# Optimization experiments

Measured on AMD Instinct MI355X. Metric: run time of the kernel, lower is better.

## Reference

```python
import jax, jax.numpy as jnp
import numpy as np

K = 8          # number of nearest neighbors (init kwarg k)
CONST = 0.1    # inverseweight const
NUM = 1.0      # inverseweight num


def setup_inputs() -> dict:
    key = jax.random.key(0)
    k1, k2 = jax.random.split(key)
    data1 = jax.random.normal(k1, (4096, 1024), dtype=jnp.float32)
    data2 = jax.random.normal(k2, (8192, 1024), dtype=jnp.float32)
    return {"data1": data1, "data2": data2}


def reference(data1, data2):
    # pairwise Euclidean distance (torch.dist with p=2): [N, M]
    x2 = jnp.sum(data1 * data1, axis=1, keepdims=True)          # [N, 1]
    y2 = jnp.sum(data2 * data2, axis=1)                         # [M]
    d2 = x2 + y2[None, :] - 2.0 * (data1 @ data2.T)             # [N, M]
    dist = jnp.sqrt(jnp.maximum(d2, 1e-12))

    # k smallest distances and their indices
    neg_top, idx = jax.lax.top_k(-dist, K)                      # [N, K]
    knn_dist = -neg_top                                         # [N, K]

    # inverse weighting: w = num / (dist + const)
    w = NUM / (knn_dist + CONST)                                # [N, K]

    # gather neighbor vectors and weighted-average them
    neigh = data2[idx]                                          # [N, K, D]
    out = jnp.einsum('nk,nkd->nd', w, neigh) / jnp.sum(w, axis=1, keepdims=True)
    return out
```

## Files before the change

kernel.cpp:

```cpp
#include <hip/hip_runtime.h>


typedef short bf16x8 __attribute__((ext_vector_type(8)));
typedef float f32x4 __attribute__((ext_vector_type(4)));

#define SENTINEL 1e30f
#define BKK 32

static __device__ __forceinline__ unsigned short f2bf(float f) {
  unsigned u = __float_as_uint(f);
  return (unsigned short)((u + 0x7fffu + ((u >> 16) & 1u)) >> 16);
}

__global__ __launch_bounds__(256) void convert_all_kernel(
    const float* __restrict__ A, const float* __restrict__ B,
    unsigned short* __restrict__ Abf, unsigned short* __restrict__ Bbf,
    float* __restrict__ y2, int N) {
  const int bid = blockIdx.x;
  const int tid = threadIdx.x;
  if (bid < N) {
    const float4 v = ((const float4*)&A[(size_t)bid * 1024])[tid];
    ushort4 o;
    o.x = f2bf(v.x); o.y = f2bf(v.y); o.z = f2bf(v.z); o.w = f2bf(v.w);
    ((ushort4*)&Abf[(size_t)bid * 1024])[tid] = o;
  } else {
    const int m = bid - N;
    __shared__ float red[256];
    const float4 v = ((const float4*)&B[(size_t)m * 1024])[tid];
    ushort4 o;
    o.x = f2bf(v.x); o.y = f2bf(v.y); o.z = f2bf(v.z); o.w = f2bf(v.w);
    ((ushort4*)&Bbf[(size_t)m * 1024])[tid] = o;
    red[tid] = v.x * v.x + v.y * v.y + v.z * v.z + v.w * v.w;
    __syncthreads();
    for (int s = 128; s > 0; s >>= 1) {
      if (tid < s) red[tid] += red[tid + s];
      __syncthreads();
    }
    if (tid == 0) y2[m] = red[0];
  }
}

#define CAS(sa, ia, sb, ib)                         \
  do {                                              \
    if ((sa) > (sb)) {                              \
      const float _t = (sa); (sa) = (sb); (sb) = _t;\
      const int _u = (ia); (ia) = (ib); (ib) = _u;  \
    }                                               \
  } while (0)

#define STAGE(sk, b)                                                          \
  do {                                                                        \
    const unsigned short* gA_ =                                               \
        Abf + (size_t)(r0 + w * 16 + srow) * 1024 + (sk) * 32 + sofs;         \
    const unsigned short* gB_ =                                               \
        Bbf + (size_t)(c0 + w * 32 + srow) * 1024 + (sk) * 32 + sofs;         \
    __builtin_amdgcn_global_load_lds(                                         \
        (const __attribute__((address_space(1))) void*)gA_,                   \
        (__attribute__((address_space(3))) void*)&As[b][(w * 16) * 32],       \
        16, 0, 0);                                                            \
    __builtin_amdgcn_global_load_lds(                                         \
        (const __attribute__((address_space(1))) void*)gB_,                   \
        (__attribute__((address_space(3))) void*)&Bs[b][(w * 32) * 32],       \
        16, 0, 0);                                                            \
    __builtin_amdgcn_global_load_lds(                                         \
        (const __attribute__((address_space(1))) void*)(gB_ + (size_t)16 * 1024), \
        (__attribute__((address_space(3))) void*)&Bs[b][(w * 32 + 16) * 32],  \
        16, 0, 0);                                                            \
  } while (0)

#define COMPUTE(b)                                                            \
  do {                                                                        \
    bf16x8 af, bfr[8];                                                        \
    af = *(const bf16x8*)&As[b][frowA * 32 + fofs];                           \
    _Pragma("unroll")                                                         \
    for (int fj = 0; fj < 8; ++fj)                                            \
      bfr[fj] = *(const bf16x8*)&Bs[b][(frowB + fj * 16) * 32 + fofs];        \
    __builtin_amdgcn_s_setprio(1);                                            \
    _Pragma("unroll")                                                         \
    for (int fj = 0; fj < 8; ++fj)                                            \
      acc[fj] = __builtin_amdgcn_mfma_f32_16x16x32_bf16(                      \
          bfr[fj], af, acc[fj], 0, 0, 0);                                     \
    __builtin_amdgcn_s_setprio(0);                                            \
  } while (0)

#define PIPE_SYNC(N)                                                          \
  do {                                                                        \
    asm volatile("s_waitcnt vmcnt(" #N ")" ::: "memory");                     \
    __builtin_amdgcn_sched_barrier(0);                                        \
    __builtin_amdgcn_s_barrier();                                             \
    __builtin_amdgcn_sched_barrier(0);                                        \
  } while (0)

__global__ __launch_bounds__(256, 4) void screen8_kernel(
    const unsigned short* __restrict__ Abf, const unsigned short* __restrict__ Bbf,
    const float* __restrict__ y2g,
    float* __restrict__ cand_s, int* __restrict__ cand_i) {
  __shared__ unsigned short As[3][64 * 32];
  __shared__ unsigned short Bs[3][128 * 32];

  const int tid = threadIdx.x;
  const int w = tid >> 6;
  const int lane = tid & 63;

  const int v = blockIdx.x + gridDim.x * blockIdx.y;
  const int u = v >> 3;
  const int window = (v & 7) * 8 + (u & 7);
  const int rowtile = u >> 3;
  const int r0 = rowtile * 64;
  const int c0 = window * 128;

  const int srow = lane >> 2;
  const int sofs = ((lane & 3) ^ ((lane >> 3) & 3)) * 8;

  const int frowA = w * 16 + (lane & 15);
  const int frowB = lane & 15;
  const int fofs = ((lane >> 4) ^ ((lane >> 1) & 3)) * 8;
  const int cgrp = (lane >> 4) * 4;

  f32x4 acc[8];
#pragma unroll
  for (int fj = 0; fj < 8; ++fj) {
    f32x4 z = {0.f, 0.f, 0.f, 0.f};
    acc[fj] = z;
  }

  STAGE(0, 0);
  STAGE(1, 1);
  int cA = 0, cB = 1, cC = 2;
  for (int t = 0; t < 31; ++t) {
    PIPE_SYNC(3);
    if (t < 30) STAGE(t + 2, cC);
    __builtin_amdgcn_sched_barrier(0);
    COMPUTE(cA);
    const int tmp = cA; cA = cB; cB = cC; cC = tmp;
  }
  PIPE_SYNC(0);
  COMPUTE(cA);

  float ls[8];
  int li[8];
#pragma unroll
  for (int j = 0; j < 8; ++j) { ls[j] = SENTINEL; li[j] = 0x7fffffff; }
  const int cb = c0 + cgrp;
#pragma unroll
  for (int fj = 0; fj < 8; ++fj) {
    const float4 y2q = *(const float4*)&y2g[c0 + fj * 16 + cgrp];
#pragma unroll
    for (int reg = 0; reg < 4; ++reg) {
      const float s = y2q[reg] - 2.0f * acc[fj][reg];
      if (s < ls[7]) {
        ls[7] = s; li[7] = cb + fj * 16 + reg;
#pragma unroll
        for (int j = 7; j > 0; --j) {
          if (ls[j] < ls[j - 1]) {
            const float t = ls[j]; ls[j] = ls[j - 1]; ls[j - 1] = t;
            const int u2 = li[j]; li[j] = li[j - 1]; li[j - 1] = u2;
          }
        }
      }
    }
  }
#pragma unroll
  for (int off = 16; off <= 32; off <<= 1) {
    float rs[8];
    int ri[8];
#pragma unroll
    for (int j = 0; j < 8; ++j) {
      rs[j] = __shfl_xor(ls[j], off, 64);
      ri[j] = __shfl_xor(li[j], off, 64);
    }
    float ms[8];
    int mi_[8];
#pragma unroll
    for (int i = 0; i < 8; ++i) {
      const bool t = ls[i] < rs[7 - i];
      ms[i] = t ? ls[i] : rs[7 - i];
      mi_[i] = t ? li[i] : ri[7 - i];
    }
    CAS(ms[0], mi_[0], ms[4], mi_[4]);
    CAS(ms[1], mi_[1], ms[5], mi_[5]);
    CAS(ms[2], mi_[2], ms[6], mi_[6]);
    CAS(ms[3], mi_[3], ms[7], mi_[7]);
    CAS(ms[0], mi_[0], ms[2], mi_[2]);
    CAS(ms[1], mi_[1], ms[3], mi_[3]);
    CAS(ms[4], mi_[4], ms[6], mi_[6]);
    CAS(ms[5], mi_[5], ms[7], mi_[7]);
    CAS(ms[0], mi_[0], ms[1], mi_[1]);
    CAS(ms[2], mi_[2], ms[3], mi_[3]);
    CAS(ms[4], mi_[4], ms[5], mi_[5]);
    CAS(ms[6], mi_[6], ms[7], mi_[7]);
#pragma unroll
    for (int j = 0; j < 8; ++j) { ls[j] = ms[j]; li[j] = mi_[j]; }
  }
  if ((lane >> 4) == 0) {
    const int row = r0 + w * 16 + lane;
    const size_t base = ((size_t)row * 64 + window) * 8;
#pragma unroll
    for (int j = 0; j < 8; ++j) {
      cand_s[base + j] = ls[j];
      cand_i[base + j] = li[j];
    }
  }
}

__global__ __launch_bounds__(256) void finalize6_kernel(
    const float* __restrict__ A, const float* __restrict__ B,
    const float* __restrict__ y2g,
    const float* __restrict__ cand_s, const int* __restrict__ cand_i,
    float* __restrict__ out) {
  const int tid = threadIdx.x;
  const int w = tid >> 6;
  const int lane = tid & 63;
  const int rloc = w >> 1;
  const int wh = w & 1;
  const int n = blockIdx.x * 2 + rloc;
  __shared__ float comb[2][2][16];

  float s12[12];
  int i12[12];
  {
    const float4* cs = (const float4*)&cand_s[(size_t)n * 512 + lane * 8];
    const int4* cj = (const int4*)&cand_i[(size_t)n * 512 + lane * 8];
    const float4 sa = cs[0], sb = cs[1];
    const int4 ja = cj[0], jb = cj[1];
    s12[0] = sa.x; s12[1] = sa.y; s12[2] = sa.z; s12[3] = sa.w;
    s12[4] = sb.x; s12[5] = sb.y; s12[6] = sb.z; s12[7] = sb.w;
    i12[0] = ja.x; i12[1] = ja.y; i12[2] = ja.z; i12[3] = ja.w;
    i12[4] = jb.x; i12[5] = jb.y; i12[6] = jb.z; i12[7] = jb.w;
#pragma unroll
    for (int j = 8; j < 12; ++j) { s12[j] = SENTINEL; i12[j] = 0x7fffffff; }
  }

#pragma unroll
  for (int off = 1; off <= 32; off <<= 1) {
    float rs[12];
    int ri[12];
#pragma unroll
    for (int j = 0; j < 12; ++j) {
      rs[j] = __shfl_xor(s12[j], off, 64);
      ri[j] = __shfl_xor(i12[j], off, 64);
    }
    float ms[12];
    int mj[12];
#pragma unroll
    for (int j = 0; j < 12; ++j) {
      const bool tke = s12[j] < rs[11 - j];
      ms[j] = tke ? s12[j] : rs[11 - j];
      mj[j] = tke ? i12[j] : ri[11 - j];
    }
    CAS(ms[0], mj[0], ms[8], mj[8]);  CAS(ms[1], mj[1], ms[9], mj[9]);
    CAS(ms[2], mj[2], ms[10], mj[10]); CAS(ms[3], mj[3], ms[11], mj[11]);
    CAS(ms[4], mj[4], ms[8], mj[8]);  CAS(ms[5], mj[5], ms[9], mj[9]);
    CAS(ms[6], mj[6], ms[10], mj[10]); CAS(ms[7], mj[7], ms[11], mj[11]);
    CAS(ms[0], mj[0], ms[2], mj[2]);  CAS(ms[1], mj[1], ms[3], mj[3]);
    CAS(ms[4], mj[4], ms[6], mj[6]);  CAS(ms[5], mj[5], ms[7], mj[7]);
    CAS(ms[8], mj[8], ms[10], mj[10]); CAS(ms[9], mj[9], ms[11], mj[11]);
    CAS(ms[0], mj[0], ms[1], mj[1]);  CAS(ms[2], mj[2], ms[3], mj[3]);
    CAS(ms[4], mj[4], ms[5], mj[5]);  CAS(ms[6], mj[6], ms[7], mj[7]);
    CAS(ms[8], mj[8], ms[9], mj[9]);  CAS(ms[10], mj[10], ms[11], mj[11]);
#pragma unroll
    for (int j = 0; j < 12; ++j) { s12[j] = ms[j]; i12[j] = mj[j]; }
  }

  const float4* Arow = (const float4*)&A[(size_t)n * 1024];
  const int fbase = wh * 128 + lane * 2;
  float4 a4[2];
  a4[0] = Arow[fbase];
  a4[1] = Arow[fbase + 1];
  float4 bk0[12], bk1[12];
#pragma unroll
  for (int j = 0; j < 12; ++j) {
    const float4* Brow = (const float4*)&B[(size_t)i12[j] * 1024];
    bk0[j] = Brow[fbase];
    bk1[j] = Brow[fbase + 1];
  }
  float part[13];
  part[12] = a4[0].x * a4[0].x + a4[0].y * a4[0].y + a4[0].z * a4[0].z +
             a4[0].w * a4[0].w + a4[1].x * a4[1].x + a4[1].y * a4[1].y +
             a4[1].z * a4[1].z + a4[1].w * a4[1].w;
#pragma unroll
  for (int j = 0; j < 12; ++j) {
    part[j] = a4[0].x * bk0[j].x + a4[0].y * bk0[j].y + a4[0].z * bk0[j].z +
              a4[0].w * bk0[j].w;
    part[j] += a4[1].x * bk1[j].x + a4[1].y * bk1[j].y + a4[1].z * bk1[j].z +
               a4[1].w * bk1[j].w;
  }
#pragma unroll
  for (int r = 0; r < 13; ++r) {
#pragma unroll
    for (int off = 32; off >= 1; off >>= 1) part[r] += __shfl_xor(part[r], off, 64);
  }
  if (lane == 0) {
#pragma unroll
    for (int r = 0; r < 13; ++r) comb[rloc][wh][r] = part[r];
  }
  __syncthreads();
  float tot[13];
#pragma unroll
  for (int r = 0; r < 13; ++r) tot[r] = comb[rloc][0][r] + comb[rloc][1][r];

  const float x2 = tot[12];
  float d2v[12];
  float wsel[12];
  bool used[12];
#pragma unroll
  for (int j = 0; j < 12; ++j) {
    d2v[j] = x2 + y2g[i12[j]] - 2.0f * tot[j];
    used[j] = false;
    wsel[j] = 0.0f;
  }
  float wsum = 0.0f;
  for (int k = 0; k < 8; ++k) {
    float bd = SENTINEL;
    int bi = 0x7fffffff, bslot = 0;
#pragma unroll
    for (int j = 0; j < 12; ++j) {
      if (used[j]) continue;
      const float d2 = d2v[j];
      if (d2 < bd || (d2 == bd && i12[j] < bi)) { bd = d2; bi = i12[j]; bslot = j; }
    }
    used[bslot] = true;
    const float d2c = fmaxf(bd, 1e-12f);
    const float wv = 1.0f / (sqrtf(d2c) + 0.1f);
    wsel[bslot] = wv;
    wsum += wv;
  }
  const float inv = 1.0f / wsum;

  float4 o0 = {0, 0, 0, 0}, o1 = {0, 0, 0, 0};
#pragma unroll
  for (int j = 0; j < 12; ++j) {
    const float wv = wsel[j];
    o0.x += wv * bk0[j].x; o0.y += wv * bk0[j].y;
    o0.z += wv * bk0[j].z; o0.w += wv * bk0[j].w;
    o1.x += wv * bk1[j].x; o1.y += wv * bk1[j].y;
    o1.z += wv * bk1[j].z; o1.w += wv * bk1[j].w;
  }
  o0.x *= inv; o0.y *= inv; o0.z *= inv; o0.w *= inv;
  o1.x *= inv; o1.y *= inv; o1.z *= inv; o1.w *= inv;
  float4* Orow = (float4*)&out[(size_t)n * 1024];
  Orow[fbase] = o0;
  Orow[fbase + 1] = o1;
}

__global__ __launch_bounds__(256) void rownorm_kernel(
    const float* __restrict__ B, float* __restrict__ y2) {
  const int m = blockIdx.x;
  const int tid = threadIdx.x;
  __shared__ float red[256];
  const float4 v = *(const float4*)&B[(size_t)m * 1024 + tid * 4];
  red[tid] = v.x * v.x + v.y * v.y + v.z * v.z + v.w * v.w;
  __syncthreads();
  for (int s = 128; s > 0; s >>= 1) {
    if (tid < s) red[tid] += red[tid + s];
    __syncthreads();
  }
  if (tid == 0) y2[m] = red[0];
}

__global__ __launch_bounds__(256) void knn_chunk_kernel(
    const float* __restrict__ A, const float* __restrict__ B,
    const float* __restrict__ y2g,
    float* __restrict__ cand_s, int* __restrict__ cand_i) {
  __shared__ float As[BKK][68];
  __shared__ float Bs[BKK][68];
  __shared__ float Sc[64][65];

  const int tid = threadIdx.x;
  const int tx = tid & 15;
  const int ty = tid >> 4;
  const int r0 = blockIdx.y * 64;
  const int c0 = blockIdx.x * 1024;
  const int lrow = tid >> 3;
  const int lk = (tid & 7) * 4;

  float top_s[8];
  int top_i[8];
#pragma unroll
  for (int j = 0; j < 8; ++j) { top_s[j] = SENTINEL; top_i[j] = 0x7fffffff; }

  for (int tile = 0; tile < 16; ++tile) {
    const int cbase = c0 + tile * 64;
    float acc[4][4];
#pragma unroll
    for (int i = 0; i < 4; ++i)
#pragma unroll
      for (int j = 0; j < 4; ++j) acc[i][j] = 0.0f;

    for (int k0 = 0; k0 < 1024; k0 += BKK) {
      const float4 a0 = *(const float4*)&A[(size_t)(r0 + lrow) * 1024 + k0 + lk];
      const float4 a1 = *(const float4*)&A[(size_t)(r0 + lrow + 32) * 1024 + k0 + lk];
      const float4 b0 = *(const float4*)&B[(size_t)(cbase + lrow) * 1024 + k0 + lk];
      const float4 b1 = *(const float4*)&B[(size_t)(cbase + lrow + 32) * 1024 + k0 + lk];
      __syncthreads();
      As[lk + 0][lrow] = a0.x; As[lk + 1][lrow] = a0.y;
      As[lk + 2][lrow] = a0.z; As[lk + 3][lrow] = a0.w;
      As[lk + 0][lrow + 32] = a1.x; As[lk + 1][lrow + 32] = a1.y;
      As[lk + 2][lrow + 32] = a1.z; As[lk + 3][lrow + 32] = a1.w;
      Bs[lk + 0][lrow] = b0.x; Bs[lk + 1][lrow] = b0.y;
      Bs[lk + 2][lrow] = b0.z; Bs[lk + 3][lrow] = b0.w;
      Bs[lk + 0][lrow + 32] = b1.x; Bs[lk + 1][lrow + 32] = b1.y;
      Bs[lk + 2][lrow + 32] = b1.z; Bs[lk + 3][lrow + 32] = b1.w;
      __syncthreads();
#pragma unroll
      for (int kk = 0; kk < BKK; ++kk) {
        const float4 av = *(const float4*)&As[kk][ty * 4];
        const float4 bv = *(const float4*)&Bs[kk][tx * 4];
        acc[0][0] += av.x * bv.x; acc[0][1] += av.x * bv.y;
        acc[0][2] += av.x * bv.z; acc[0][3] += av.x * bv.w;
        acc[1][0] += av.y * bv.x; acc[1][1] += av.y * bv.y;
        acc[1][2] += av.y * bv.z; acc[1][3] += av.y * bv.w;
        acc[2][0] += av.z * bv.x; acc[2][1] += av.z * bv.y;
        acc[2][2] += av.z * bv.z; acc[2][3] += av.z * bv.w;
        acc[3][0] += av.w * bv.x; acc[3][1] += av.w * bv.y;
        acc[3][2] += av.w * bv.z; acc[3][3] += av.w * bv.w;
      }
    }
#pragma unroll
    for (int i = 0; i < 4; ++i) {
      const int row = ty * 4 + i;
#pragma unroll
      for (int j = 0; j < 4; ++j) {
        const int col = tx * 4 + j;
        Sc[row][col] = y2g[cbase + col] - 2.0f * acc[i][j];
      }
    }
    __syncthreads();
    if (tid < 64) {
      for (int c = 0; c < 64; ++c) {
        const float s = Sc[tid][c];
        if (s < top_s[7]) {
          top_s[7] = s; top_i[7] = cbase + c;
#pragma unroll
          for (int j = 7; j > 0; --j) {
            if (top_s[j] < top_s[j - 1]) {
              const float tss = top_s[j]; top_s[j] = top_s[j - 1]; top_s[j - 1] = tss;
              const int tii = top_i[j]; top_i[j] = top_i[j - 1]; top_i[j - 1] = tii;
            }
          }
        }
      }
    }
  }

  if (tid < 64) {
    const int n = r0 + tid;
    const int base = (n * gridDim.x + blockIdx.x) * 8;
#pragma unroll
    for (int j = 0; j < 8; ++j) {
      cand_s[base + j] = top_s[j];
      cand_i[base + j] = top_i[j];
    }
  }
}

__global__ __launch_bounds__(256) void finalize_kernel(
    const float* __restrict__ A, const float* __restrict__ B,
    const float* __restrict__ cand_s, const int* __restrict__ cand_i,
    float* __restrict__ out, int nchunks) {
  const int n = blockIdx.x;
  const int tid = threadIdx.x;
  __shared__ float red[256];
  __shared__ float ls[64];
  __shared__ int li[64];
  __shared__ float wsh2[8];
  __shared__ int wid[8];
  __shared__ float wsum_sh;

  const int ncand = nchunks * 8;
  const float4 a = *(const float4*)&A[(size_t)n * 1024 + tid * 4];
  red[tid] = a.x * a.x + a.y * a.y + a.z * a.z + a.w * a.w;
  if (tid < ncand) {
    ls[tid] = cand_s[n * ncand + tid];
    li[tid] = cand_i[n * ncand + tid];
  }
  __syncthreads();
  for (int s = 128; s > 0; s >>= 1) {
    if (tid < s) red[tid] += red[tid + s];
    __syncthreads();
  }
  if (tid == 0) {
    const float x2 = red[0];
    float wsum = 0.0f;
    for (int j = 0; j < 8; ++j) {
      float bs = SENTINEL;
      int bi = 0x7fffffff;
      int bp = 0;
      for (int c = 0; c < ncand; ++c) {
        const float s_ = ls[c];
        const int i_ = li[c];
        if (s_ < bs || (s_ == bs && i_ < bi)) { bs = s_; bi = i_; bp = c; }
      }
      ls[bp] = SENTINEL; li[bp] = 0x7fffffff;
      float d2 = x2 + bs;
      d2 = fmaxf(d2, 1e-12f);
      const float wkk = 1.0f / (sqrtf(d2) + 0.1f);
      wsh2[j] = wkk; wid[j] = bi;
      wsum += wkk;
    }
    wsum_sh = wsum;
  }
  __syncthreads();
  const float inv = 1.0f / wsum_sh;
  float ox = 0.0f, oy = 0.0f, oz = 0.0f, ow = 0.0f;
#pragma unroll
  for (int j = 0; j < 8; ++j) {
    const float wkk = wsh2[j];
    const float4 v = *(const float4*)&B[(size_t)wid[j] * 1024 + tid * 4];
    ox += wkk * v.x; oy += wkk * v.y; oz += wkk * v.z; ow += wkk * v.w;
  }
  float4 o;
  o.x = ox * inv; o.y = oy * inv; o.z = oz * inv; o.w = ow * inv;
  *(float4*)&out[(size_t)n * 1024 + tid * 4] = o;
}

extern "C" void kernel_launch(void* const* d_in, const int* in_sizes, int n_in,
                              void* d_out, int out_size, void* d_ws, size_t ws_size,
                              hipStream_t stream) {
  const float* A = (const float*)d_in[0];
  const float* Bm = (const float*)d_in[1];
  const int D = 1024;
  const int N = in_sizes[0] / D;
  const int M = in_sizes[1] / D;

  const size_t needA = (size_t)N * D * 2;
  const size_t needB = (size_t)M * D * 2;
  const size_t needC = (size_t)N * 512 * 4;
  const size_t need = needA + needB + (size_t)M * 4 + 2 * needC;

  if (ws_size >= need && M == 8192 && N % 64 == 0 && N % 2 == 0) {
    unsigned short* Abf = (unsigned short*)d_ws;
    unsigned short* Bbf = Abf + (size_t)N * D;
    float* y2 = (float*)(Bbf + (size_t)M * D);
    float* cand_s = y2 + M;
    int* cand_i = (int*)(cand_s + (size_t)N * 512);

    convert_all_kernel<<<N + M, 256, 0, stream>>>(A, Bm, Abf, Bbf, y2, N);
    dim3 g(64, N / 64);
    screen8_kernel<<<g, 256, 0, stream>>>(Abf, Bbf, y2, cand_s, cand_i);
    finalize6_kernel<<<N / 2, 256, 0, stream>>>(A, Bm, y2, cand_s, cand_i,
                                                (float*)d_out);
  } else {
    float* y2 = (float*)d_ws;
    float* cand_s = y2 + M;
    int* cand_i = (int*)(cand_s + (size_t)N * 64);
    rownorm_kernel<<<M, 256, 0, stream>>>(Bm, y2);
    dim3 gridB(M / 1024, N / 64);
    knn_chunk_kernel<<<gridB, 256, 0, stream>>>(A, Bm, y2, cand_s, cand_i);
    finalize_kernel<<<N, 256, 0, stream>>>(A, Bm, cand_s, cand_i, (float*)d_out, M / 1024);
  }
}
```

Baseline: 314.3 us.

## Double row tile to 128 and switch screening GEMM to 32x32x16 MFMA

```diff
diff --git a/kernel.cpp b/kernel.cpp
--- a/kernel.cpp
+++ b/kernel.cpp
@@ -3,6 +3,7 @@
 
 typedef short bf16x8 __attribute__((ext_vector_type(8)));
 typedef float f32x4 __attribute__((ext_vector_type(4)));
+typedef float f32x16 __attribute__((ext_vector_type(16)));
 
 #define SENTINEL 1e30f
 #define BKK 32
@@ -51,12 +52,16 @@
 #define STAGE(sk, b)                                                          \
   do {                                                                        \
     const unsigned short* gA_ =                                               \
-        Abf + (size_t)(r0 + w * 16 + srow) * 1024 + (sk) * 32 + sofs;         \
+        Abf + (size_t)(r0 + w * 32 + srow) * 1024 + (sk) * 32 + sofs;         \
     const unsigned short* gB_ =                                               \
         Bbf + (size_t)(c0 + w * 32 + srow) * 1024 + (sk) * 32 + sofs;         \
     __builtin_amdgcn_global_load_lds(                                         \
         (const __attribute__((address_space(1))) void*)gA_,                   \
-        (__attribute__((address_space(3))) void*)&As[b][(w * 16) * 32],       \
+        (__attribute__((address_space(3))) void*)&As[b][(w * 32) * 32],       \
+        16, 0, 0);                                                            \
+    __builtin_amdgcn_global_load_lds(                                         \
+        (const __attribute__((address_space(1))) void*)(gA_ + (size_t)16 * 1024), \
+        (__attribute__((address_space(3))) void*)&As[b][(w * 32 + 16) * 32],  \
         16, 0, 0);                                                            \
     __builtin_amdgcn_global_load_lds(                                         \
         (const __attribute__((address_space(1))) void*)gB_,                   \
@@ -70,16 +75,26 @@
 
 #define COMPUTE(b)                                                            \
   do {                                                                        \
-    bf16x8 af, bfr[8];                                                        \
-    af = *(const bf16x8*)&As[b][frowA * 32 + fofs];                           \
-    _Pragma("unroll")                                                         \
-    for (int fj = 0; fj < 8; ++fj)                                            \
-      bfr[fj] = *(const bf16x8*)&Bs[b][(frowB + fj * 16) * 32 + fofs];        \
+    bf16x8 af0, af1, bf00, bf01, bf10, bf11, bf20, bf21, bf30, bf31;          \
+    af0 = *(const bf16x8*)&As[b][(w * 32 + rr) * 32 + fofs0];                 \
+    af1 = *(const bf16x8*)&As[b][(w * 32 + rr) * 32 + fofs1];                 \
+    bf00 = *(const bf16x8*)&Bs[b][(0 * 32 + rr) * 32 + fofs0];                \
+    bf01 = *(const bf16x8*)&Bs[b][(0 * 32 + rr) * 32 + fofs1];                \
+    bf10 = *(const bf16x8*)&Bs[b][(1 * 32 + rr) * 32 + fofs0];                \
+    bf11 = *(const bf16x8*)&Bs[b][(1 * 32 + rr) * 32 + fofs1];                \
+    bf20 = *(const bf16x8*)&Bs[b][(2 * 32 + rr) * 32 + fofs0];                \
+    bf21 = *(const bf16x8*)&Bs[b][(2 * 32 + rr) * 32 + fofs1];                \
+    bf30 = *(const bf16x8*)&Bs[b][(3 * 32 + rr) * 32 + fofs0];                \
+    bf31 = *(const bf16x8*)&Bs[b][(3 * 32 + rr) * 32 + fofs1];                \
     __builtin_amdgcn_s_setprio(1);                                            \
-    _Pragma("unroll")                                                         \
-    for (int fj = 0; fj < 8; ++fj)                                            \
-      acc[fj] = __builtin_amdgcn_mfma_f32_16x16x32_bf16(                      \
-          bfr[fj], af, acc[fj], 0, 0, 0);                                     \
+    acc[0] = __builtin_amdgcn_mfma_f32_32x32x16_bf16(bf00, af0, acc[0], 0, 0, 0); \
+    acc[1] = __builtin_amdgcn_mfma_f32_32x32x16_bf16(bf10, af0, acc[1], 0, 0, 0); \
+    acc[2] = __builtin_amdgcn_mfma_f32_32x32x16_bf16(bf20, af0, acc[2], 0, 0, 0); \
+    acc[3] = __builtin_amdgcn_mfma_f32_32x32x16_bf16(bf30, af0, acc[3], 0, 0, 0); \
+    acc[0] = __builtin_amdgcn_mfma_f32_32x32x16_bf16(bf01, af1, acc[0], 0, 0, 0); \
+    acc[1] = __builtin_amdgcn_mfma_f32_32x32x16_bf16(bf11, af1, acc[1], 0, 0, 0); \
+    acc[2] = __builtin_amdgcn_mfma_f32_32x32x16_bf16(bf21, af1, acc[2], 0, 0, 0); \
+    acc[3] = __builtin_amdgcn_mfma_f32_32x32x16_bf16(bf31, af1, acc[3], 0, 0, 0); \
     __builtin_amdgcn_s_setprio(0);                                            \
   } while (0)
 
@@ -91,11 +106,11 @@
     __builtin_amdgcn_sched_barrier(0);                                        \
   } while (0)
 
-__global__ __launch_bounds__(256, 4) void screen8_kernel(
+__global__ __launch_bounds__(256) void screen9_kernel(
     const unsigned short* __restrict__ Abf, const unsigned short* __restrict__ Bbf,
     const float* __restrict__ y2g,
     float* __restrict__ cand_s, int* __restrict__ cand_i) {
-  __shared__ unsigned short As[3][64 * 32];
+  __shared__ unsigned short As[3][128 * 32];
   __shared__ unsigned short Bs[3][128 * 32];
 
   const int tid = threadIdx.x;
@@ -103,24 +118,25 @@
   const int lane = tid & 63;
 
   const int v = blockIdx.x + gridDim.x * blockIdx.y;
-  const int u = v >> 3;
-  const int window = (v & 7) * 8 + (u & 7);
-  const int rowtile = u >> 3;
-  const int r0 = rowtile * 64;
+  const int window = (v & 7) * 8 + ((v >> 3) & 7);
+  const int rowtile = v >> 6;
+  const int r0 = rowtile * 128;
   const int c0 = window * 128;
 
   const int srow = lane >> 2;
   const int sofs = ((lane & 3) ^ ((lane >> 3) & 3)) * 8;
 
-  const int frowA = w * 16 + (lane & 15);
-  const int frowB = lane & 15;
-  const int fofs = ((lane >> 4) ^ ((lane >> 1) & 3)) * 8;
-  const int cgrp = (lane >> 4) * 4;
-
-  f32x4 acc[8];
-#pragma unroll
-  for (int fj = 0; fj < 8; ++fj) {
-    f32x4 z = {0.f, 0.f, 0.f, 0.f};
+  const int rr = lane & 31;
+  const int hi = lane >> 5;
+  const int q2 = (lane >> 1) & 3;
+  const int fofs0 = ((0 * 2 + hi) ^ q2) * 8;
+  const int fofs1 = ((1 * 2 + hi) ^ q2) * 8;
+
+  f32x16 acc[4];
+#pragma unroll
+  for (int fj = 0; fj < 4; ++fj) {
+    f32x16 z = {0.f, 0.f, 0.f, 0.f, 0.f, 0.f, 0.f, 0.f,
+                0.f, 0.f, 0.f, 0.f, 0.f, 0.f, 0.f, 0.f};
     acc[fj] = z;
   }
 
@@ -128,7 +144,7 @@
   STAGE(1, 1);
   int cA = 0, cB = 1, cC = 2;
   for (int t = 0; t < 31; ++t) {
-    PIPE_SYNC(3);
+    PIPE_SYNC(4);
     if (t < 30) STAGE(t + 2, cC);
     __builtin_amdgcn_sched_barrier(0);
     COMPUTE(cA);
@@ -141,15 +157,18 @@
   int li[8];
 #pragma unroll
   for (int j = 0; j < 8; ++j) { ls[j] = SENTINEL; li[j] = 0x7fffffff; }
-  const int cb = c0 + cgrp;
-#pragma unroll
-  for (int fj = 0; fj < 8; ++fj) {
-    const float4 y2q = *(const float4*)&y2g[c0 + fj * 16 + cgrp];
-#pragma unroll
-    for (int reg = 0; reg < 4; ++reg) {
-      const float s = y2q[reg] - 2.0f * acc[fj][reg];
+#pragma unroll
+  for (int fj = 0; fj < 4; ++fj) {
+    const int cb = c0 + fj * 32 + 4 * hi;
+    float4 y2q[4];
+#pragma unroll
+    for (int q = 0; q < 4; ++q)
+      y2q[q] = *(const float4*)&y2g[cb + 8 * q];
+#pragma unroll
+    for (int reg = 0; reg < 16; ++reg) {
+      const float s = y2q[reg >> 2][reg & 3] - 2.0f * acc[fj][reg];
       if (s < ls[7]) {
-        ls[7] = s; li[7] = cb + fj * 16 + reg;
+        ls[7] = s; li[7] = cb + (reg & 3) + 8 * (reg >> 2);
 #pragma unroll
         for (int j = 7; j > 0; --j) {
           if (ls[j] < ls[j - 1]) {
@@ -160,14 +179,13 @@
       }
     }
   }
-#pragma unroll
-  for (int off = 16; off <= 32; off <<= 1) {
+  {
     float rs[8];
     int ri[8];
 #pragma unroll
     for (int j = 0; j < 8; ++j) {
-      rs[j] = __shfl_xor(ls[j], off, 64);
-      ri[j] = __shfl_xor(li[j], off, 64);
+      rs[j] = __shfl_xor(ls[j], 32, 64);
+      ri[j] = __shfl_xor(li[j], 32, 64);
     }
     float ms[8];
     int mi_[8];
@@ -192,8 +210,8 @@
 #pragma unroll
     for (int j = 0; j < 8; ++j) { ls[j] = ms[j]; li[j] = mi_[j]; }
   }
-  if ((lane >> 4) == 0) {
-    const int row = r0 + w * 16 + lane;
+  if (lane < 32) {
+    const int row = r0 + w * 32 + lane;
     const size_t base = ((size_t)row * 64 + window) * 8;
 #pragma unroll
     for (int j = 0; j < 8; ++j) {
@@ -528,7 +546,7 @@
   const size_t needC = (size_t)N * 512 * 4;
   const size_t need = needA + needB + (size_t)M * 4 + 2 * needC;
 
-  if (ws_size >= need && M == 8192 && N % 64 == 0 && N % 2 == 0) {
+  if (ws_size >= need && M == 8192 && N % 128 == 0 && N % 2 == 0) {
     unsigned short* Abf = (unsigned short*)d_ws;
     unsigned short* Bbf = Abf + (size_t)N * D;
     float* y2 = (float*)(Bbf + (size_t)M * D);
@@ -536,8 +554,8 @@
     int* cand_i = (int*)(cand_s + (size_t)N * 512);
 
     convert_all_kernel<<<N + M, 256, 0, stream>>>(A, Bm, Abf, Bbf, y2, N);
-    dim3 g(64, N / 64);
-    screen8_kernel<<<g, 256, 0, stream>>>(Abf, Bbf, y2, cand_s, cand_i);
+    dim3 g(64, N / 128);
+    screen9_kernel<<<g, 256, 0, stream>>>(Abf, Bbf, y2, cand_s, cand_i);
     finalize6_kernel<<<N / 2, 256, 0, stream>>>(A, Bm, y2, cand_s, cand_i,
                                                 (float*)d_out);
   } else {
```

Result: slower. 348.1 us (+10.7%).

## Enlarge screening tile to 128x128 with two MFMA row fragments per wave

Applied to the files above, without the earlier changes.

```diff
diff --git a/kernel.cpp b/kernel.cpp
--- a/kernel.cpp
+++ b/kernel.cpp
@@ -51,12 +51,16 @@
 #define STAGE(sk, b)                                                          \
   do {                                                                        \
     const unsigned short* gA_ =                                               \
-        Abf + (size_t)(r0 + w * 16 + srow) * 1024 + (sk) * 32 + sofs;         \
+        Abf + (size_t)(r0 + w * 32 + srow) * 1024 + (sk) * 32 + sofs;         \
     const unsigned short* gB_ =                                               \
         Bbf + (size_t)(c0 + w * 32 + srow) * 1024 + (sk) * 32 + sofs;         \
     __builtin_amdgcn_global_load_lds(                                         \
         (const __attribute__((address_space(1))) void*)gA_,                   \
-        (__attribute__((address_space(3))) void*)&As[b][(w * 16) * 32],       \
+        (__attribute__((address_space(3))) void*)&As[b][(w * 32) * 32],       \
+        16, 0, 0);                                                            \
+    __builtin_amdgcn_global_load_lds(                                         \
+        (const __attribute__((address_space(1))) void*)(gA_ + (size_t)16 * 1024), \
+        (__attribute__((address_space(3))) void*)&As[b][(w * 32 + 16) * 32],  \
         16, 0, 0);                                                            \
     __builtin_amdgcn_global_load_lds(                                         \
         (const __attribute__((address_space(1))) void*)gB_,                   \
@@ -70,16 +74,20 @@
 
 #define COMPUTE(b)                                                            \
   do {                                                                        \
-    bf16x8 af, bfr[8];                                                        \
-    af = *(const bf16x8*)&As[b][frowA * 32 + fofs];                           \
+    bf16x8 af[2], bfr[8];                                                     \
+    _Pragma("unroll")                                                         \
+    for (int fi = 0; fi < 2; ++fi)                                            \
+      af[fi] = *(const bf16x8*)&As[b][(frowA + fi * 16) * 32 + fofs];         \
     _Pragma("unroll")                                                         \
     for (int fj = 0; fj < 8; ++fj)                                            \
       bfr[fj] = *(const bf16x8*)&Bs[b][(frowB + fj * 16) * 32 + fofs];        \
     __builtin_amdgcn_s_setprio(1);                                            \
     _Pragma("unroll")                                                         \
-    for (int fj = 0; fj < 8; ++fj)                                            \
-      acc[fj] = __builtin_amdgcn_mfma_f32_16x16x32_bf16(                      \
-          bfr[fj], af, acc[fj], 0, 0, 0);                                     \
+    for (int fi = 0; fi < 2; ++fi)                                            \
+      _Pragma("unroll")                                                       \
+      for (int fj = 0; fj < 8; ++fj)                                          \
+        acc[fi][fj] = __builtin_amdgcn_mfma_f32_16x16x32_bf16(                \
+            bfr[fj], af[fi], acc[fi][fj], 0, 0, 0);                           \
     __builtin_amdgcn_s_setprio(0);                                            \
   } while (0)
 
@@ -91,114 +99,128 @@
     __builtin_amdgcn_sched_barrier(0);                                        \
   } while (0)
 
-__global__ __launch_bounds__(256, 4) void screen8_kernel(
+__global__ __launch_bounds__(256) void screen10_kernel(
     const unsigned short* __restrict__ Abf, const unsigned short* __restrict__ Bbf,
     const float* __restrict__ y2g,
     float* __restrict__ cand_s, int* __restrict__ cand_i) {
-  __shared__ unsigned short As[3][64 * 32];
+  __shared__ unsigned short As[3][128 * 32];
   __shared__ unsigned short Bs[3][128 * 32];
 
   const int tid = threadIdx.x;
   const int w = tid >> 6;
   const int lane = tid & 63;
 
-  const int v = blockIdx.x + gridDim.x * blockIdx.y;
-  const int u = v >> 3;
-  const int window = (v & 7) * 8 + (u & 7);
-  const int rowtile = u >> 3;
-  const int r0 = rowtile * 64;
+  const int bx = blockIdx.x;
+  const int window = (bx & 7) * 8 + ((bx >> 3) & 7);
+  const int r0 = blockIdx.y * 128;
   const int c0 = window * 128;
 
   const int srow = lane >> 2;
   const int sofs = ((lane & 3) ^ ((lane >> 3) & 3)) * 8;
 
-  const int frowA = w * 16 + (lane & 15);
+  const int frowA = w * 32 + (lane & 15);
   const int frowB = lane & 15;
   const int fofs = ((lane >> 4) ^ ((lane >> 1) & 3)) * 8;
   const int cgrp = (lane >> 4) * 4;
 
-  f32x4 acc[8];
-#pragma unroll
-  for (int fj = 0; fj < 8; ++fj) {
-    f32x4 z = {0.f, 0.f, 0.f, 0.f};
-    acc[fj] = z;
-  }
+  f32x4 acc[2][8];
+#pragma unroll
+  for (int fi = 0; fi < 2; ++fi)
+#pragma unroll
+    for (int fj = 0; fj < 8; ++fj) {
+      f32x4 z = {0.f, 0.f, 0.f, 0.f};
+      acc[fi][fj] = z;
+    }
 
   STAGE(0, 0);
   STAGE(1, 1);
-  int cA = 0, cB = 1, cC = 2;
-  for (int t = 0; t < 31; ++t) {
-    PIPE_SYNC(3);
-    if (t < 30) STAGE(t + 2, cC);
+  int t = 0;
+#pragma unroll 1
+  for (int it = 0; it < 10; ++it) {
+    PIPE_SYNC(4);
+    STAGE(t + 2, 2);
     __builtin_amdgcn_sched_barrier(0);
-    COMPUTE(cA);
-    const int tmp = cA; cA = cB; cB = cC; cC = tmp;
-  }
+    COMPUTE(0);
+    PIPE_SYNC(4);
+    STAGE(t + 3, 0);
+    __builtin_amdgcn_sched_barrier(0);
+    COMPUTE(1);
+    PIPE_SYNC(4);
+    STAGE(t + 4, 1);
+    __builtin_amdgcn_sched_barrier(0);
+    COMPUTE(2);
+    t += 3;
+  }
+  PIPE_SYNC(4);
+  COMPUTE(0);
   PIPE_SYNC(0);
-  COMPUTE(cA);
-
-  float ls[8];
-  int li[8];
-#pragma unroll
-  for (int j = 0; j < 8; ++j) { ls[j] = SENTINEL; li[j] = 0x7fffffff; }
-  const int cb = c0 + cgrp;
-#pragma unroll
-  for (int fj = 0; fj < 8; ++fj) {
-    const float4 y2q = *(const float4*)&y2g[c0 + fj * 16 + cgrp];
-#pragma unroll
-    for (int reg = 0; reg < 4; ++reg) {
-      const float s = y2q[reg] - 2.0f * acc[fj][reg];
-      if (s < ls[7]) {
-        ls[7] = s; li[7] = cb + fj * 16 + reg;
-#pragma unroll
-        for (int j = 7; j > 0; --j) {
-          if (ls[j] < ls[j - 1]) {
-            const float t = ls[j]; ls[j] = ls[j - 1]; ls[j - 1] = t;
-            const int u2 = li[j]; li[j] = li[j - 1]; li[j - 1] = u2;
+  COMPUTE(1);
+
+#pragma unroll
+  for (int fi = 0; fi < 2; ++fi) {
+    float ls[8];
+    int li[8];
+#pragma unroll
+    for (int j = 0; j < 8; ++j) { ls[j] = SENTINEL; li[j] = 0x7fffffff; }
+    const int cb = c0 + cgrp;
+#pragma unroll
+    for (int fj = 0; fj < 8; ++fj) {
+      const float4 y2q = *(const float4*)&y2g[c0 + fj * 16 + cgrp];
+#pragma unroll
+      for (int reg = 0; reg < 4; ++reg) {
+        const float s = y2q[reg] - 2.0f * acc[fi][fj][reg];
+        if (s < ls[7]) {
+          ls[7] = s; li[7] = cb + fj * 16 + reg;
+#pragma unroll
+          for (int j = 7; j > 0; --j) {
+            if (ls[j] < ls[j - 1]) {
+              const float tt = ls[j]; ls[j] = ls[j - 1]; ls[j - 1] = tt;
+              const int u2 = li[j]; li[j] = li[j - 1]; li[j - 1] = u2;
+            }
           }
         }
       }
     }
-  }
-#pragma unroll
-  for (int off = 16; off <= 32; off <<= 1) {
-    float rs[8];
-    int ri[8];
-#pragma unroll
-    for (int j = 0; j < 8; ++j) {
-      rs[j] = __shfl_xor(ls[j], off, 64);
-      ri[j] = __shfl_xor(li[j], off, 64);
-    }
-    float ms[8];
-    int mi_[8];
-#pragma unroll
-    for (int i = 0; i < 8; ++i) {
-      const bool t = ls[i] < rs[7 - i];
-      ms[i] = t ? ls[i] : rs[7 - i];
-      mi_[i] = t ? li[i] : ri[7 - i];
-    }
-    CAS(ms[0], mi_[0], ms[4], mi_[4]);
-    CAS(ms[1], mi_[1], ms[5], mi_[5]);
-    CAS(ms[2], mi_[2], ms[6], mi_[6]);
-    CAS(ms[3], mi_[3], ms[7], mi_[7]);
-    CAS(ms[0], mi_[0], ms[2], mi_[2]);
-    CAS(ms[1], mi_[1], ms[3], mi_[3]);
-    CAS(ms[4], mi_[4], ms[6], mi_[6]);
-    CAS(ms[5], mi_[5], ms[7], mi_[7]);
-    CAS(ms[0], mi_[0], ms[1], mi_[1]);
-    CAS(ms[2], mi_[2], ms[3], mi_[3]);
-    CAS(ms[4], mi_[4], ms[5], mi_[5]);
-    CAS(ms[6], mi_[6], ms[7], mi_[7]);
-#pragma unroll
-    for (int j = 0; j < 8; ++j) { ls[j] = ms[j]; li[j] = mi_[j]; }
-  }
-  if ((lane >> 4) == 0) {
-    const int row = r0 + w * 16 + lane;
-    const size_t base = ((size_t)row * 64 + window) * 8;
-#pragma unroll
-    for (int j = 0; j < 8; ++j) {
-      cand_s[base + j] = ls[j];
-      cand_i[base + j] = li[j];
+#pragma unroll
+    for (int off = 16; off <= 32; off <<= 1) {
+      float rs[8];
+      int ri[8];
+#pragma unroll
+      for (int j = 0; j < 8; ++j) {
+        rs[j] = __shfl_xor(ls[j], off, 64);
+        ri[j] = __shfl_xor(li[j], off, 64);
+      }
+      float ms[8];
+      int mi_[8];
+#pragma unroll
+      for (int i = 0; i < 8; ++i) {
+        const bool tk = ls[i] < rs[7 - i];
+        ms[i] = tk ? ls[i] : rs[7 - i];
+        mi_[i] = tk ? li[i] : ri[7 - i];
+      }
+      CAS(ms[0], mi_[0], ms[4], mi_[4]);
+      CAS(ms[1], mi_[1], ms[5], mi_[5]);
+      CAS(ms[2], mi_[2], ms[6], mi_[6]);
+      CAS(ms[3], mi_[3], ms[7], mi_[7]);
+      CAS(ms[0], mi_[0], ms[2], mi_[2]);
+      CAS(ms[1], mi_[1], ms[3], mi_[3]);
+      CAS(ms[4], mi_[4], ms[6], mi_[6]);
+      CAS(ms[5], mi_[5], ms[7], mi_[7]);
+      CAS(ms[0], mi_[0], ms[1], mi_[1]);
+      CAS(ms[2], mi_[2], ms[3], mi_[3]);
+      CAS(ms[4], mi_[4], ms[5], mi_[5]);
+      CAS(ms[6], mi_[6], ms[7], mi_[7]);
+#pragma unroll
+      for (int j = 0; j < 8; ++j) { ls[j] = ms[j]; li[j] = mi_[j]; }
+    }
+    if ((lane >> 4) == 0) {
+      const int row = r0 + w * 32 + fi * 16 + lane;
+      const size_t base = ((size_t)row * 64 + window) * 8;
+#pragma unroll
+      for (int j = 0; j < 8; ++j) {
+        cand_s[base + j] = ls[j];
+        cand_i[base + j] = li[j];
+      }
     }
   }
 }
@@ -528,7 +550,7 @@
   const size_t needC = (size_t)N * 512 * 4;
   const size_t need = needA + needB + (size_t)M * 4 + 2 * needC;
 
-  if (ws_size >= need && M == 8192 && N % 64 == 0 && N % 2 == 0) {
+  if (ws_size >= need && M == 8192 && N % 128 == 0 && N % 2 == 0) {
     unsigned short* Abf = (unsigned short*)d_ws;
     unsigned short* Bbf = Abf + (size_t)N * D;
     float* y2 = (float*)(Bbf + (size_t)M * D);
@@ -536,8 +558,8 @@
     int* cand_i = (int*)(cand_s + (size_t)N * 512);
 
     convert_all_kernel<<<N + M, 256, 0, stream>>>(A, Bm, Abf, Bbf, y2, N);
-    dim3 g(64, N / 64);
-    screen8_kernel<<<g, 256, 0, stream>>>(Abf, Bbf, y2, cand_s, cand_i);
+    dim3 g(64, N / 128);
+    screen10_kernel<<<g, 256, 0, stream>>>(Abf, Bbf, y2, cand_s, cand_i);
     finalize6_kernel<<<N / 2, 256, 0, stream>>>(A, Bm, y2, cand_s, cand_i,
                                                 (float*)d_out);
   } else {
```

Result: slower. 397.4 us (+26.4%).
